# Kernel tuning notes

Hardware: AMD Instinct MI355X
Metric: run time of the kernel (lower is better)

Reference implementation:

```python
import jax, jax.numpy as jnp
import numpy as np

B, I, D = 2048, 4096, 512          # batch of candidates, num rated items, item_dim
IE, UE = 512, 1024                 # item_emb, user_emb
D1, D2, D3 = 1024, 512, 256        # MLP dense widths


def setup_inputs() -> dict:
    key = jax.random.key(0)
    ks = jax.random.split(key, 16)
    s = 0.02  # weight init scale
    candidate_items = jax.random.normal(ks[0], (B, D), dtype=jnp.float32)
    rated_items = jax.random.normal(ks[1], (I, D), dtype=jnp.float32)
    ratings = jax.random.uniform(ks[2], (B, I), dtype=jnp.float32, minval=0.5, maxval=5.0)
    keep = jax.random.uniform(ks[3], (B, I)) < 0.05
    user_matrix = jnp.where(keep, ratings, 0.0)
    return dict(
        candidate_items=candidate_items,
        rated_items=rated_items,
        user_matrix=user_matrix,
        att_w=jax.random.normal(ks[4], (2 * D, 1), dtype=jnp.float32) * s,
        att_b=jnp.zeros((1,), jnp.float32),
        iw1=jax.random.normal(ks[5], (D, 2 * IE), dtype=jnp.float32) * s,
        ib1=jnp.zeros((2 * IE,), jnp.float32),
        iw2=jax.random.normal(ks[6], (2 * IE, IE), dtype=jnp.float32) * s,
        ib2=jnp.zeros((IE,), jnp.float32),
        uw1=jax.random.normal(ks[7], (D, 2 * UE), dtype=jnp.float32) * s,
        ub1=jnp.zeros((2 * UE,), jnp.float32),
        uw2=jax.random.normal(ks[8], (2 * UE, UE), dtype=jnp.float32) * s,
        ub2=jnp.zeros((UE,), jnp.float32),
        mw1=jax.random.normal(ks[9], (IE + UE, D1), dtype=jnp.float32) * s,
        mb1=jnp.zeros((D1,), jnp.float32),
        mw2=jax.random.normal(ks[10], (D1, D2), dtype=jnp.float32) * s,
        mb2=jnp.zeros((D2,), jnp.float32),
        mw3=jax.random.normal(ks[11], (D2, D3), dtype=jnp.float32) * s,
        mb3=jnp.zeros((D3,), jnp.float32),
        mw4=jax.random.normal(ks[12], (D3, 1), dtype=jnp.float32) * s,
        mb4=jnp.zeros((1,), jnp.float32),
    )


def reference(candidate_items, rated_items, user_matrix,
              att_w, att_b, iw1, ib1, iw2, ib2, uw1, ub1, uw2, ub2,
              mw1, mb1, mw2, mb2, mw3, mb3, mw4, mb4):
    d = candidate_items.shape[1]
    # AttentionNet(Linear(2D,1)) on cat(cand_repeat, rated_tile) decomposes exactly:
    # score[b,i] = cand[b] @ w_c + rated[i] @ w_r + b  (same math, no (B*I,2D) blowup)
    wc, wr = att_w[:d], att_w[d:]                      # (D,1), (D,1)
    scores = candidate_items @ wc + (rated_items @ wr).T + att_b  # (B, I)
    scores = jnp.where(user_matrix == 0.0, -jnp.inf, scores)
    att = jax.nn.softmax(scores, axis=1)
    att = jnp.nan_to_num(att, nan=0.0, posinf=0.0, neginf=0.0)  # rows with no ratings -> 0
    user_feat = (att * user_matrix) @ rated_items      # (B, D)
    # dual towers (dropout = identity in eval)
    item_emb = jax.nn.relu(jax.nn.relu(candidate_items @ iw1 + ib1) @ iw2 + ib2)
    user_emb = jax.nn.relu(jax.nn.relu(user_feat @ uw1 + ub1) @ uw2 + ub2)
    x = jnp.concatenate([item_emb, user_emb], axis=1)  # (B, IE+UE)
    x = jax.nn.relu(x @ mw1 + mb1)
    x = jax.nn.relu(x @ mw2 + mb2)
    x = jax.nn.relu(x @ mw3 + mb3)
    return x @ mw4 + mb4                               # (B, 1)
```

## Files before the change

### kernel.cpp

```cpp
#include <hip/hip_runtime.h>
#include <cstddef>

constexpr int Bn = 2048;
constexpr int In = 4096;
constexpr int Dn = 512;

typedef _Float16 f16;
typedef _Float16 f16x8 __attribute__((ext_vector_type(8)));
typedef float    f32x4 __attribute__((ext_vector_type(4)));

__device__ __forceinline__ void gld16(const f16* g, f16* l) {
  __builtin_amdgcn_global_load_lds(
      (const __attribute__((address_space(1))) void*)g,
      (__attribute__((address_space(3))) void*)l, 16, 0, 0);
}

__global__ __launch_bounds__(256) void k_rs(const float* __restrict__ rated,
                                            const float* __restrict__ att_w,
                                            float* __restrict__ rs) {
  const int wid  = threadIdx.x >> 6;
  const int lane = threadIdx.x & 63;
  const int i = blockIdx.x * 4 + wid;
  const float* row = rated + (size_t)i * Dn;
  const float* wr  = att_w + Dn;
  float s = 0.f;
  #pragma unroll
  for (int d = 0; d < Dn / 64; ++d)
    s = fmaf(row[lane + d * 64], wr[lane + d * 64], s);
  #pragma unroll
  for (int off = 32; off > 0; off >>= 1) s += __shfl_down(s, off);
  if (lane == 0) rs[i] = s;
}

struct PrepDesc { const float* src; f16* dst; int K, N, nt, isCast; };
struct PrepPack { PrepDesc d[9]; };

__global__ __launch_bounds__(256) void k_attprep(const float* __restrict__ um,
                                                 const float* __restrict__ rs,
                                                 f16* __restrict__ att,
                                                 PrepPack pk) {
  __shared__ float smem[4100];
  const int tid = threadIdx.x;

  if ((int)blockIdx.x >= Bn) {
    int local = blockIdx.x - Bn;
    int q = 0;
    while (local >= pk.d[q].nt) { local -= pk.d[q].nt; ++q; }
    const PrepDesc dd = pk.d[q];
    if (dd.isCast) {
      const int i = (local * 256 + tid) * 4;
      const float4 v = *reinterpret_cast<const float4*>(dd.src + i);
      f16* p = dd.dst + i;
      p[0] = (f16)v.x; p[1] = (f16)v.y; p[2] = (f16)v.z; p[3] = (f16)v.w;
      return;
    }
    float (*tile)[33] = reinterpret_cast<float (*)[33]>(smem);
    const int tx = tid & 31;
    const int ty = tid >> 5;
    const int n0 = (local % (dd.N / 32)) * 32;
    const int k0 = (local / (dd.N / 32)) * 32;
    #pragma unroll
    for (int i = 0; i < 4; ++i)
      tile[ty + i * 8][tx] = dd.src[(size_t)(k0 + ty + i * 8) * dd.N + n0 + tx];
    __syncthreads();
    #pragma unroll
    for (int i = 0; i < 4; ++i)
      dd.dst[(size_t)(n0 + ty + i * 8) * dd.K + k0 + tx] = (f16)tile[tx][ty + i * 8];
    return;
  }

  float* t = smem;
  float* red = smem + 4096;
  const int b = blockIdx.x;
  const float* umrow = um + (size_t)b * In;

  float ua[16];
  float lmax = -INFINITY;
  #pragma unroll
  for (int it = 0; it < 4; ++it) {
    const int i = (it * 256 + tid) * 4;
    const float4 v = *reinterpret_cast<const float4*>(umrow + i);
    ua[it * 4 + 0] = v.x; ua[it * 4 + 1] = v.y;
    ua[it * 4 + 2] = v.z; ua[it * 4 + 3] = v.w;
    #pragma unroll
    for (int j = 0; j < 4; ++j) {
      if (ua[it * 4 + j] != 0.f) {
        const float r = rs[i + j];
        t[i + j] = r;
        lmax = fmaxf(lmax, r);
      } else {
        t[i + j] = -INFINITY;
      }
    }
  }
  #pragma unroll
  for (int off = 32; off > 0; off >>= 1) lmax = fmaxf(lmax, __shfl_down(lmax, off));
  if ((tid & 63) == 0) red[tid >> 6] = lmax;
  __syncthreads();
  const float m = fmaxf(fmaxf(red[0], red[1]), fmaxf(red[2], red[3]));
  __syncthreads();

  float lsum = 0.f;
  #pragma unroll
  for (int it = 0; it < 4; ++it) {
    const int i = (it * 256 + tid) * 4;
    #pragma unroll
    for (int j = 0; j < 4; ++j) {
      float v = 0.f;
      if (ua[it * 4 + j] != 0.f) {
        const float e = __expf(t[i + j] - m);
        lsum += e;
        v = e * ua[it * 4 + j];
      }
      t[i + j] = v;
    }
  }
  #pragma unroll
  for (int off = 32; off > 0; off >>= 1) lsum += __shfl_down(lsum, off);
  if ((tid & 63) == 0) red[tid >> 6] = lsum;
  __syncthreads();
  const float S = red[0] + red[1] + red[2] + red[3];
  const float inv = (S > 0.f) ? 1.0f / S : 0.0f;

  f16* arow = att + (size_t)b * In;
  #pragma unroll
  for (int it = 0; it < 2; ++it) {
    const int i = (it * 256 + tid) * 8;
    f16x8 h;
    #pragma unroll
    for (int j = 0; j < 8; ++j) h[j] = (f16)(t[i + j] * inv);
    *reinterpret_cast<f16x8*>(arow + i) = h;
  }
}

struct GemmDesc {
  const f16* A;
  const f16* Wt;
  const float* bias;
  f16* C;
  int K, ldc, relu;
};

__global__ __launch_bounds__(256, 2) void k_mgemm(GemmDesc dA, GemmDesc dB, int bSplit) {
  __shared__ __align__(16) f16 As[64 * 64];
  __shared__ __align__(16) f16 Bs[64 * 64];

  const bool second = ((int)blockIdx.x >= bSplit);
  const GemmDesc d = second ? dB : dA;
  const int local = second ? (int)blockIdx.x - bSplit : (int)blockIdx.x;

  const int bm = (local & 31) * 64;
  const int bn = (local >> 5) * 64;

  const int tid  = threadIdx.x;
  const int lane = tid & 63;
  const int wave = tid >> 6;
  const int wrow = (wave >> 1) * 32;
  const int wcol = (wave & 1) * 32;
  const int lrow = lane & 15;
  const int koff = (lane >> 4) * 8;

  const int c0   = wave * 2;
  const int rgrp = lane >> 3;
  const int colh = (lane & 7) * 8;

  const f16* gA0 = d.A  + (size_t)(bm + c0 * 8 + rgrp) * d.K + colh;
  const f16* gA1 = d.A  + (size_t)(bm + c0 * 8 + 8 + rgrp) * d.K + colh;
  const f16* gB0 = d.Wt + (size_t)(bn + c0 * 8 + rgrp) * d.K + colh;
  const f16* gB1 = d.Wt + (size_t)(bn + c0 * 8 + 8 + rgrp) * d.K + colh;
  f16* lA0 = &As[(c0 + 0) * 512];
  f16* lA1 = &As[(c0 + 1) * 512];
  f16* lB0 = &Bs[(c0 + 0) * 512];
  f16* lB1 = &Bs[(c0 + 1) * 512];

  f32x4 acc[2][2] = {};

  for (int k0 = 0; k0 < d.K; k0 += 64) {
    gld16(gA0 + k0, lA0);
    gld16(gA1 + k0, lA1);
    gld16(gB0 + k0, lB0);
    gld16(gB1 + k0, lB1);
    __syncthreads();

    #pragma unroll
    for (int kss = 0; kss < 2; ++kss) {
      const int kk = kss * 32 + koff;
      const f16x8 a0 = *reinterpret_cast<const f16x8*>(&As[(wrow +  0 + lrow) * 64 + kk]);
      const f16x8 a1 = *reinterpret_cast<const f16x8*>(&As[(wrow + 16 + lrow) * 64 + kk]);
      const f16x8 b0 = *reinterpret_cast<const f16x8*>(&Bs[(wcol +  0 + lrow) * 64 + kk]);
      const f16x8 b1 = *reinterpret_cast<const f16x8*>(&Bs[(wcol + 16 + lrow) * 64 + kk]);

      acc[0][0] = __builtin_amdgcn_mfma_f32_16x16x32_f16(a0, b0, acc[0][0], 0, 0, 0);
      acc[0][1] = __builtin_amdgcn_mfma_f32_16x16x32_f16(a0, b1, acc[0][1], 0, 0, 0);
      acc[1][0] = __builtin_amdgcn_mfma_f32_16x16x32_f16(a1, b0, acc[1][0], 0, 0, 0);
      acc[1][1] = __builtin_amdgcn_mfma_f32_16x16x32_f16(a1, b1, acc[1][1], 0, 0, 0);
    }
    __syncthreads();
  }

  const int orow = (lane >> 4) * 4;
  #pragma unroll
  for (int mf = 0; mf < 2; ++mf)
    #pragma unroll
    for (int nf = 0; nf < 2; ++nf) {
      const int col = bn + wcol + nf * 16 + lrow;
      const float bv = d.bias ? d.bias[col] : 0.f;
      #pragma unroll
      for (int rr = 0; rr < 4; ++rr) {
        const int row = bm + wrow + mf * 16 + orow + rr;
        float v = acc[mf][nf][rr] + bv;
        if (d.relu) v = fmaxf(v, 0.f);
        d.C[(size_t)row * d.ldc + col] = (f16)v;
      }
    }
}

__global__ __launch_bounds__(256) void k_tail(const f16* __restrict__ h2,
                                              const f16* __restrict__ t_mw3,
                                              const float* __restrict__ mb3,
                                              const float* __restrict__ mw4,
                                              const float* __restrict__ mb4,
                                              float* __restrict__ out) {
  __shared__ f16 rows[4][512];
  __shared__ float red[4][4];
  const int tid = threadIdx.x;
  const int r0 = blockIdx.x * 4;

  *reinterpret_cast<f16x8*>(&rows[tid >> 6][(tid & 63) * 8]) =
      *reinterpret_cast<const f16x8*>(&h2[(size_t)(r0 + (tid >> 6)) * 512 + (tid & 63) * 8]);
  __syncthreads();

  const int j = tid;
  float acc[4] = {};
  for (int k = 0; k < 512; k += 8) {
    const f16x8 w = *reinterpret_cast<const f16x8*>(&t_mw3[(size_t)j * 512 + k]);
    #pragma unroll
    for (int e = 0; e < 8; ++e) {
      const float wf = (float)w[e];
      #pragma unroll
      for (int r = 0; r < 4; ++r)
        acc[r] = fmaf(wf, (float)rows[r][k + e], acc[r]);
    }
  }
  const float b3 = mb3[j];
  const float m4 = mw4[j];
  const int lane = tid & 63;
  const int wid  = tid >> 6;
  #pragma unroll
  for (int r = 0; r < 4; ++r) {
    float v = fmaxf(acc[r] + b3, 0.f) * m4;
    #pragma unroll
    for (int off = 32; off > 0; off >>= 1) v += __shfl_down(v, off);
    if (lane == 0) red[r][wid] = v;
  }
  __syncthreads();
  if (tid < 4)
    out[r0 + tid] = red[tid][0] + red[tid][1] + red[tid][2] + red[tid][3] + mb4[0];
}

extern "C" void kernel_launch(void* const* d_in, const int* in_sizes, int n_in,
                              void* d_out, int out_size, void* d_ws, size_t ws_size,
                              hipStream_t stream) {
  const float* cand  = (const float*)d_in[0];
  const float* rated = (const float*)d_in[1];
  const float* um    = (const float*)d_in[2];
  const float* att_w = (const float*)d_in[3];
  const float* iw1 = (const float*)d_in[5];
  const float* ib1 = (const float*)d_in[6];
  const float* iw2 = (const float*)d_in[7];
  const float* ib2 = (const float*)d_in[8];
  const float* uw1 = (const float*)d_in[9];
  const float* ub1 = (const float*)d_in[10];
  const float* uw2 = (const float*)d_in[11];
  const float* ub2 = (const float*)d_in[12];
  const float* mw1 = (const float*)d_in[13];
  const float* mb1 = (const float*)d_in[14];
  const float* mw2 = (const float*)d_in[15];
  const float* mb2 = (const float*)d_in[16];
  const float* mw3 = (const float*)d_in[17];
  const float* mb3 = (const float*)d_in[18];
  const float* mw4 = (const float*)d_in[19];
  const float* mb4 = (const float*)d_in[20];
  float* out = (float*)d_out;

  f16*   hws = (f16*)d_ws;
  float* rs  = (float*)d_ws;
  size_t off = 8192;
  auto take = [&](size_t n) { f16* p = hws + off; off += n; return p; };
  f16* t_iw1   = take(512 * 1024);
  f16* t_iw2   = take(1024 * 512);
  f16* t_uw1   = take(512 * 2048);
  f16* t_uw2   = take(2048 * 1024);
  f16* t_mw1   = take(1536 * 1024);
  f16* t_mw2   = take(1024 * 512);
  f16* t_mw3   = take(512 * 256);
  f16* t_rated = take(512 * 4096);
  f16* cand_h  = take(2048 * 512);
  f16* uf_h    = take(2048 * 512);
  f16* att_d   = take(2048 * 4096);
  f16* h_i1    = take(2048 * 1024);
  f16* Xc      = take(2048 * 1536);
  f16* h_u1 = att_d;
  f16* h_m1 = h_i1;
  f16* h_m2 = uf_h;

  dim3 blk(256);

  k_rs<<<dim3(In / 4), blk, 0, stream>>>(rated, att_w, rs);

  PrepPack pk = {{
      { rated, t_rated, 4096,  512, (512/32)*(4096/32), 0 },
      { iw1,   t_iw1,    512, 1024, (1024/32)*(512/32), 0 },
      { iw2,   t_iw2,   1024,  512, (512/32)*(1024/32), 0 },
      { uw1,   t_uw1,    512, 2048, (2048/32)*(512/32), 0 },
      { uw2,   t_uw2,   2048, 1024, (1024/32)*(2048/32), 0 },
      { mw1,   t_mw1,   1536, 1024, (1024/32)*(1536/32), 0 },
      { mw2,   t_mw2,   1024,  512, (512/32)*(1024/32), 0 },
      { mw3,   t_mw3,    512,  256, (256/32)*(512/32), 0 },
      { cand,  cand_h,     0,    0, (Bn * Dn) / 1024, 1 },
  }};
  int prepGrid = 0;
  for (int q = 0; q < 9; ++q) prepGrid += pk.d[q].nt;
  k_attprep<<<dim3(Bn + prepGrid), blk, 0, stream>>>(um, rs, att_d, pk);

  GemmDesc dUF = { att_d,  t_rated, nullptr, uf_h,     4096,  512, 0 };
  GemmDesc dI1 = { cand_h, t_iw1,   ib1,     h_i1,      512, 1024, 1 };
  GemmDesc dU1 = { uf_h,   t_uw1,   ub1,     h_u1,      512, 2048, 1 };
  GemmDesc dI2 = { h_i1,   t_iw2,   ib2,     Xc,       1024, 1536, 1 };
  GemmDesc dU2 = { h_u1,   t_uw2,   ub2,     Xc + 512, 2048, 1536, 1 };
  GemmDesc dM1 = { Xc,     t_mw1,   mb1,     h_m1,     1536, 1024, 1 };
  GemmDesc dM2 = { h_m1,   t_mw2,   mb2,     h_m2,     1024,  512, 1 };

  k_mgemm<<<dim3(768), blk, 0, stream>>>(dUF, dI1, 256);
  k_mgemm<<<dim3(1280), blk, 0, stream>>>(dU1, dI2, 1024);
  k_mgemm<<<dim3(512), blk, 0, stream>>>(dU2, dU2, 512);
  k_mgemm<<<dim3(512), blk, 0, stream>>>(dM1, dM1, 512);
  k_mgemm<<<dim3(256), blk, 0, stream>>>(dM2, dM2, 256);

  k_tail<<<dim3(Bn / 4), blk, 0, stream>>>(h_m2, t_mw3, mb3, mw4, mb4, out);
}
```

Baseline: 300.7 us.

## Double-buffer LDS, swizzle tiles, and split-K the attention-weighted user-feature GEMM

The generic MFMA GEMM now double-buffers its LDS tiles so the next K-slab's global-to-LDS loads are issued while the current slab is computed. It also XOR-swizzles the LDS layout to cut bank conflicts on the fragment reads. The K=4096 user-feature GEMM is split four ways along K, writing fp32 partials that a new reduce kernel sums and converts to fp16. This raises block count and occupancy for that GEMM, at the cost of an extra launch and partial-sum traffic through global memory.

```diff
diff --git a/kernel.cpp b/kernel.cpp
--- a/kernel.cpp
+++ b/kernel.cpp
@@ -138,19 +138,23 @@
   const f16* Wt;
   const float* bias;
   f16* C;
-  int K, ldc, relu;
+  float* P;
+  int K, Kc, ldc, nTilesN, relu;
 };
 
 __global__ __launch_bounds__(256, 2) void k_mgemm(GemmDesc dA, GemmDesc dB, int bSplit) {
-  __shared__ __align__(16) f16 As[64 * 64];
-  __shared__ __align__(16) f16 Bs[64 * 64];
+  __shared__ __align__(16) f16 As[2][64 * 64];
+  __shared__ __align__(16) f16 Bs[2][64 * 64];
 
   const bool second = ((int)blockIdx.x >= bSplit);
   const GemmDesc d = second ? dB : dA;
   const int local = second ? (int)blockIdx.x - bSplit : (int)blockIdx.x;
 
   const int bm = (local & 31) * 64;
-  const int bn = (local >> 5) * 64;
+  const int rest = local >> 5;
+  const int bn = (rest % d.nTilesN) * 64;
+  const int ks = rest / d.nTilesN;
+  const size_t kBeg = (size_t)ks * d.Kc;
 
   const int tid  = threadIdx.x;
   const int lane = tid & 63;
@@ -158,37 +162,46 @@
   const int wrow = (wave >> 1) * 32;
   const int wcol = (wave & 1) * 32;
   const int lrow = lane & 15;
-  const int koff = (lane >> 4) * 8;
-
-  const int c0   = wave * 2;
-  const int rgrp = lane >> 3;
-  const int colh = (lane & 7) * 8;
-
-  const f16* gA0 = d.A  + (size_t)(bm + c0 * 8 + rgrp) * d.K + colh;
-  const f16* gA1 = d.A  + (size_t)(bm + c0 * 8 + 8 + rgrp) * d.K + colh;
-  const f16* gB0 = d.Wt + (size_t)(bn + c0 * 8 + rgrp) * d.K + colh;
-  const f16* gB1 = d.Wt + (size_t)(bn + c0 * 8 + 8 + rgrp) * d.K + colh;
-  f16* lA0 = &As[(c0 + 0) * 512];
-  f16* lA1 = &As[(c0 + 1) * 512];
-  f16* lB0 = &Bs[(c0 + 0) * 512];
-  f16* lB1 = &Bs[(c0 + 1) * 512];
+
+  const int c0    = wave * 2;
+  const int rgrp  = lane >> 3;
+  const int sslot = lane & 7;
+  const int scol  = ((sslot ^ rgrp) * 8);
+
+  const f16* gA0 = d.A  + (size_t)(bm + c0 * 8 + rgrp) * d.K + kBeg + scol;
+  const f16* gA1 = d.A  + (size_t)(bm + c0 * 8 + 8 + rgrp) * d.K + kBeg + scol;
+  const f16* gB0 = d.Wt + (size_t)(bn + c0 * 8 + rgrp) * d.K + kBeg + scol;
+  const f16* gB1 = d.Wt + (size_t)(bn + c0 * 8 + 8 + rgrp) * d.K + kBeg + scol;
+  const int lA0 = (c0 + 0) * 512;
+  const int lA1 = (c0 + 1) * 512;
+
+  #define STAGE(buf, k0)                                   \
+    gld16(gA0 + (k0), &As[buf][lA0]);                      \
+    gld16(gA1 + (k0), &As[buf][lA1]);                      \
+    gld16(gB0 + (k0), &Bs[buf][lA0]);                      \
+    gld16(gB1 + (k0), &Bs[buf][lA1]);
+
+  const int r7 = lrow & 7;
+  const int sw0 = ((0 * 4 + (lane >> 4)) ^ r7) * 8;
+  const int sw1 = ((1 * 4 + (lane >> 4)) ^ r7) * 8;
 
   f32x4 acc[2][2] = {};
 
-  for (int k0 = 0; k0 < d.K; k0 += 64) {
-    gld16(gA0 + k0, lA0);
-    gld16(gA1 + k0, lA1);
-    gld16(gB0 + k0, lB0);
-    gld16(gB1 + k0, lB1);
-    __syncthreads();
-
+  STAGE(0, 0);
+  __syncthreads();
+  int cur = 0;
+  for (int k0 = 0; k0 < d.Kc; k0 += 64) {
+    if (k0 + 64 < d.Kc) { STAGE(cur ^ 1, k0 + 64); }
+
+    const f16* A_ = As[cur];
+    const f16* B_ = Bs[cur];
     #pragma unroll
     for (int kss = 0; kss < 2; ++kss) {
-      const int kk = kss * 32 + koff;
-      const f16x8 a0 = *reinterpret_cast<const f16x8*>(&As[(wrow +  0 + lrow) * 64 + kk]);
-      const f16x8 a1 = *reinterpret_cast<const f16x8*>(&As[(wrow + 16 + lrow) * 64 + kk]);
-      const f16x8 b0 = *reinterpret_cast<const f16x8*>(&Bs[(wcol +  0 + lrow) * 64 + kk]);
-      const f16x8 b1 = *reinterpret_cast<const f16x8*>(&Bs[(wcol + 16 + lrow) * 64 + kk]);
+      const int sw = kss ? sw1 : sw0;
+      const f16x8 a0 = *reinterpret_cast<const f16x8*>(&A_[(wrow +  0 + lrow) * 64 + sw]);
+      const f16x8 a1 = *reinterpret_cast<const f16x8*>(&A_[(wrow + 16 + lrow) * 64 + sw]);
+      const f16x8 b0 = *reinterpret_cast<const f16x8*>(&B_[(wcol +  0 + lrow) * 64 + sw]);
+      const f16x8 b1 = *reinterpret_cast<const f16x8*>(&B_[(wcol + 16 + lrow) * 64 + sw]);
 
       acc[0][0] = __builtin_amdgcn_mfma_f32_16x16x32_f16(a0, b0, acc[0][0], 0, 0, 0);
       acc[0][1] = __builtin_amdgcn_mfma_f32_16x16x32_f16(a0, b1, acc[0][1], 0, 0, 0);
@@ -196,23 +209,73 @@
       acc[1][1] = __builtin_amdgcn_mfma_f32_16x16x32_f16(a1, b1, acc[1][1], 0, 0, 0);
     }
     __syncthreads();
-  }
+    cur ^= 1;
+  }
+  #undef STAGE
 
   const int orow = (lane >> 4) * 4;
-  #pragma unroll
-  for (int mf = 0; mf < 2; ++mf)
-    #pragma unroll
-    for (int nf = 0; nf < 2; ++nf) {
-      const int col = bn + wcol + nf * 16 + lrow;
-      const float bv = d.bias ? d.bias[col] : 0.f;
+  if (d.P) {
+    const int N = d.nTilesN * 64;
+    float* pp = d.P + (size_t)ks * ((size_t)2048 * N);
+    #pragma unroll
+    for (int mf = 0; mf < 2; ++mf)
       #pragma unroll
-      for (int rr = 0; rr < 4; ++rr) {
-        const int row = bm + wrow + mf * 16 + orow + rr;
-        float v = acc[mf][nf][rr] + bv;
-        if (d.relu) v = fmaxf(v, 0.f);
-        d.C[(size_t)row * d.ldc + col] = (f16)v;
+      for (int nf = 0; nf < 2; ++nf) {
+        const int col = bn + wcol + nf * 16 + lrow;
+        #pragma unroll
+        for (int rr = 0; rr < 4; ++rr) {
+          const int row = bm + wrow + mf * 16 + orow + rr;
+          pp[(size_t)row * N + col] = acc[mf][nf][rr];
+        }
       }
-    }
+  } else {
+    #pragma unroll
+    for (int mf = 0; mf < 2; ++mf)
+      #pragma unroll
+      for (int nf = 0; nf < 2; ++nf) {
+        const int col = bn + wcol + nf * 16 + lrow;
+        const float bv = d.bias ? d.bias[col] : 0.f;
+        #pragma unroll
+        for (int rr = 0; rr < 4; ++rr) {
+          const int row = bm + wrow + mf * 16 + orow + rr;
+          float v = acc[mf][nf][rr] + bv;
+          if (d.relu) v = fmaxf(v, 0.f);
+          d.C[(size_t)row * d.ldc + col] = (f16)v;
+        }
+      }
+  }
+}
+
+__global__ __launch_bounds__(256) void k_reduce(const float* __restrict__ P,
+                                                int S, int MN, int N,
+                                                const float* __restrict__ bias,
+                                                int relu, f16* __restrict__ C,
+                                                int ldc) {
+  const int idx = (blockIdx.x * 256 + threadIdx.x) * 8;
+  float v[8];
+  {
+    const float4 a0 = *reinterpret_cast<const float4*>(P + idx);
+    const float4 a1 = *reinterpret_cast<const float4*>(P + idx + 4);
+    v[0] = a0.x; v[1] = a0.y; v[2] = a0.z; v[3] = a0.w;
+    v[4] = a1.x; v[5] = a1.y; v[6] = a1.z; v[7] = a1.w;
+  }
+  for (int s = 1; s < S; ++s) {
+    const float* ps = P + (size_t)s * MN + idx;
+    const float4 b0 = *reinterpret_cast<const float4*>(ps);
+    const float4 b1 = *reinterpret_cast<const float4*>(ps + 4);
+    v[0] += b0.x; v[1] += b0.y; v[2] += b0.z; v[3] += b0.w;
+    v[4] += b1.x; v[5] += b1.y; v[6] += b1.z; v[7] += b1.w;
+  }
+  const int row = idx / N;
+  const int col = idx % N;
+  f16x8 h;
+  #pragma unroll
+  for (int j = 0; j < 8; ++j) {
+    float x = v[j] + (bias ? bias[col + j] : 0.f);
+    if (relu) x = fmaxf(x, 0.f);
+    h[j] = (f16)x;
+  }
+  *reinterpret_cast<f16x8*>(C + (size_t)row * ldc + col) = h;
 }
 
 __global__ __launch_bounds__(256) void k_tail(const f16* __restrict__ h2,
@@ -300,6 +363,7 @@
   f16* att_d   = take(2048 * 4096);
   f16* h_i1    = take(2048 * 1024);
   f16* Xc      = take(2048 * 1536);
+  float* Pbuf  = (float*)take(4 * 2048 * 512 * 2);
   f16* h_u1 = att_d;
   f16* h_m1 = h_i1;
   f16* h_m2 = uf_h;
@@ -323,15 +387,17 @@
   for (int q = 0; q < 9; ++q) prepGrid += pk.d[q].nt;
   k_attprep<<<dim3(Bn + prepGrid), blk, 0, stream>>>(um, rs, att_d, pk);
 
-  GemmDesc dUF = { att_d,  t_rated, nullptr, uf_h,     4096,  512, 0 };
-  GemmDesc dI1 = { cand_h, t_iw1,   ib1,     h_i1,      512, 1024, 1 };
-  GemmDesc dU1 = { uf_h,   t_uw1,   ub1,     h_u1,      512, 2048, 1 };
-  GemmDesc dI2 = { h_i1,   t_iw2,   ib2,     Xc,       1024, 1536, 1 };
-  GemmDesc dU2 = { h_u1,   t_uw2,   ub2,     Xc + 512, 2048, 1536, 1 };
-  GemmDesc dM1 = { Xc,     t_mw1,   mb1,     h_m1,     1536, 1024, 1 };
-  GemmDesc dM2 = { h_m1,   t_mw2,   mb2,     h_m2,     1024,  512, 1 };
-
-  k_mgemm<<<dim3(768), blk, 0, stream>>>(dUF, dI1, 256);
+  GemmDesc dUF = { att_d,  t_rated, nullptr, nullptr,  Pbuf,   4096, 1024,  512,  8, 0 };
+  GemmDesc dI1 = { cand_h, t_iw1,   ib1,     h_i1,     nullptr, 512,  512, 1024, 16, 1 };
+  GemmDesc dU1 = { uf_h,   t_uw1,   ub1,     h_u1,     nullptr, 512,  512, 2048, 32, 1 };
+  GemmDesc dI2 = { h_i1,   t_iw2,   ib2,     Xc,       nullptr, 1024, 1024, 1536, 8, 1 };
+  GemmDesc dU2 = { h_u1,   t_uw2,   ub2,     Xc + 512, nullptr, 2048, 2048, 1536, 16, 1 };
+  GemmDesc dM1 = { Xc,     t_mw1,   mb1,     h_m1,     nullptr, 1536, 1536, 1024, 16, 1 };
+  GemmDesc dM2 = { h_m1,   t_mw2,   mb2,     h_m2,     nullptr, 1024, 1024,  512,  8, 1 };
+
+  k_mgemm<<<dim3(1536), blk, 0, stream>>>(dUF, dI1, 1024);
+  k_reduce<<<dim3(512), blk, 0, stream>>>(Pbuf, 4, 2048 * 512, 512, nullptr, 0, uf_h, 512);
+
   k_mgemm<<<dim3(1280), blk, 0, stream>>>(dU1, dI2, 1024);
   k_mgemm<<<dim3(512), blk, 0, stream>>>(dU2, dU2, 512);
   k_mgemm<<<dim3(512), blk, 0, stream>>>(dM1, dM1, 512);
```

Measured after the change: 272.8 us. -9.3%, faster.
